# Kernel tuning notes

Measured on AMD Instinct MI355X. Metric: run time of the kernel, lower is better.

Reference implementation:

```python
import jax, jax.numpy as jnp
import numpy as np

_PADE_B = np.array([6.476475253248e+16, 3.238237626624e+16, 7771770303897600.0,
                    1187353796428800.0, 129060195264000.0, 10559470521600.0,
                    670442572800.0, 33522128640.0, 1323241920.0, 40840800.0,
                    960960.0, 16380.0, 182.0, 1.0])
_MAXNORM = 5.371920351148152
_MAX_SQUARINGS = 6  # randn 3x3 has Fro norm ~3 < maxnorm; 6 steps is ample headroom


def _expm(A):
    """Batched scaling-and-squaring Pade-13 matrix exponential. A: [N, d, d]."""
    b = _PADE_B.astype(A.dtype)
    d = A.shape[-1]
    ident = jnp.eye(d, dtype=A.dtype)
    fro = jnp.sqrt(jnp.sum(A * A, axis=(1, 2), keepdims=True))  # [N,1,1]
    n_sq = jnp.maximum(0.0, jnp.ceil(jnp.log2(fro / _MAXNORM)))
    Ascaled = A / (2.0 ** n_sq)
    n_sq_i = n_sq.reshape(-1).astype(jnp.int32)  # [N]

    A2 = Ascaled @ Ascaled
    A4 = A2 @ A2
    A6 = A4 @ A2
    U = Ascaled @ (A6 @ (b[13] * A6 + b[11] * A4 + b[9] * A2)
                   + b[7] * A6 + b[5] * A4 + b[3] * A2 + b[1] * ident)
    V = (A6 @ (b[12] * A6 + b[10] * A4 + b[8] * A2)
         + b[6] * A6 + b[4] * A4 + b[2] * A2 + b[0] * ident)
    P = U + V
    Q = -U + V
    R = jnp.linalg.solve(Q, P)  # torch.solve(P, Q): Q X = P

    def body(k, R):
        R2 = R @ R
        return jnp.where((k < n_sq_i)[:, None, None], R2, R)

    return jax.lax.fori_loop(0, _MAX_SQUARINGS, body, R, unroll=True)


def setup_inputs() -> dict:
    key = jax.random.key(0)
    k1, k2, k3 = jax.random.split(key, 3)
    bs, n, d = 65536, 24, 3
    return {
        "mean": jax.random.normal(k1, (bs, n, d), dtype=jnp.float32),
        "var": jax.random.normal(k2, (bs, n, d, d), dtype=jnp.float32),
        "gt": jax.random.normal(k3, (bs, n, d), dtype=jnp.float32),
    }


def reference(mean, var, gt):
    bs, n, d = mean.shape
    A = var.reshape(bs * n, d, d)
    E = _expm(A)                               # [bs*n, d, d]
    delta = (gt - mean).reshape(bs * n, d)     # [bs*n, d]
    quad = jnp.einsum('ni,nij,nj->n', delta, E, delta)
    dets = jnp.linalg.det(A)
    per = 0.5 * (quad + dets) / n              # [bs*n]
    loss = per.reshape(bs, n).sum(axis=1)      # [bs]
    return loss.mean()
```

## Files before the change

### kernel.cpp

```cpp
#include <hip/hip_runtime.h>

#define TPB 256

#define B0  6.476475253248e+16f
#define B1  3.238237626624e+16f
#define B2  7.7717703038976e+15f
#define B3  1.1873537964288e+15f
#define B4  1.29060195264e+14f
#define B5  1.05594705216e+13f
#define B6  6.704425728e+11f
#define B7  3.352212864e+10f
#define B8  1.32324192e+9f
#define B9  4.08408e+7f
#define B10 9.6096e+5f
#define B11 1.638e+4f
#define B12 182.0f
#define B13 1.0f

__device__ __forceinline__ void mm3(const float a[9], const float b[9], float c[9]) {
#pragma unroll
  for (int i = 0; i < 3; ++i) {
#pragma unroll
    for (int j = 0; j < 3; ++j) {
      c[i * 3 + j] = fmaf(a[i * 3 + 0], b[0 + j],
                     fmaf(a[i * 3 + 1], b[3 + j],
                          a[i * 3 + 2] * b[6 + j]));
    }
  }
}

__global__ __launch_bounds__(TPB, 4) void expm_loss_kernel(
    const float* __restrict__ mean, const float* __restrict__ var,
    const float* __restrict__ gt, float* __restrict__ partials) {
  const int tid = threadIdx.x;
  const long long i = (long long)blockIdx.x * TPB + tid;

  const float* av = var + i * 9;
  const float* mv = mean + i * 3;
  const float* gv = gt + i * 3;

  float A[9];
#pragma unroll
  for (int k = 0; k < 9; ++k) A[k] = av[k];
  const float d0 = gv[0] - mv[0];
  const float d1 = gv[1] - mv[1];
  const float d2 = gv[2] - mv[2];

  const float detA = A[0] * (A[4] * A[8] - A[5] * A[7])
                   - A[1] * (A[3] * A[8] - A[5] * A[6])
                   + A[2] * (A[3] * A[7] - A[4] * A[6]);
  float fro2 = 0.f;
#pragma unroll
  for (int k = 0; k < 9; ++k) fro2 = fmaf(A[k], A[k], fro2);
  const float nsqf = fmaxf(0.0f, ceilf(fmaf(0.5f, __log2f(fro2), -2.4253625f)));
  int nsq = (int)nsqf;
  nsq = nsq > 6 ? 6 : nsq;
  const float scl = exp2f(-nsqf);

  float As[9];
#pragma unroll
  for (int k = 0; k < 9; ++k) As[k] = A[k] * scl;

  float A2[9], A4[9], A6[9];
  mm3(As, As, A2);
  mm3(A2, A2, A4);
  mm3(A4, A2, A6);

  float W[9], T[9], U[9], V[9];
#pragma unroll
  for (int k = 0; k < 9; ++k)
    W[k] = fmaf(B13, A6[k], fmaf(B11, A4[k], B9 * A2[k]));
  mm3(A6, W, T);
#pragma unroll
  for (int k = 0; k < 9; ++k)
    T[k] = fmaf(B7, A6[k], fmaf(B5, A4[k], fmaf(B3, A2[k], T[k])));
  T[0] += B1; T[4] += B1; T[8] += B1;
  mm3(As, T, U);

#pragma unroll
  for (int k = 0; k < 9; ++k)
    W[k] = fmaf(B12, A6[k], fmaf(B10, A4[k], B8 * A2[k]));
  mm3(A6, W, V);
#pragma unroll
  for (int k = 0; k < 9; ++k)
    V[k] = fmaf(B6, A6[k], fmaf(B4, A4[k], fmaf(B2, A2[k], V[k])));
  V[0] += B0; V[4] += B0; V[8] += B0;

  const float s = 1.0f / B0;
  float P[9], Q[9];
#pragma unroll
  for (int k = 0; k < 9; ++k) {
    P[k] = (U[k] + V[k]) * s;
    Q[k] = (V[k] - U[k]) * s;
  }

  const float c00 = Q[4] * Q[8] - Q[5] * Q[7];
  const float c01 = Q[5] * Q[6] - Q[3] * Q[8];
  const float c02 = Q[3] * Q[7] - Q[4] * Q[6];
  const float c10 = Q[2] * Q[7] - Q[1] * Q[8];
  const float c11 = Q[0] * Q[8] - Q[2] * Q[6];
  const float c12 = Q[1] * Q[6] - Q[0] * Q[7];
  const float c20 = Q[1] * Q[5] - Q[2] * Q[4];
  const float c21 = Q[2] * Q[3] - Q[0] * Q[5];
  const float c22 = Q[0] * Q[4] - Q[1] * Q[3];
  const float detQ = Q[0] * c00 + Q[1] * c01 + Q[2] * c02;
  const float inv = 1.0f / detQ;
  const float Qi[9] = { c00 * inv, c10 * inv, c20 * inv,
                        c01 * inv, c11 * inv, c21 * inv,
                        c02 * inv, c12 * inv, c22 * inv };
  float R[9];
  mm3(Qi, P, R);

  for (int k = 0; k < nsq; ++k) {
    float R2[9];
    mm3(R, R, R2);
#pragma unroll
    for (int j = 0; j < 9; ++j) R[j] = R2[j];
  }

  const float t0 = fmaf(R[0], d0, fmaf(R[1], d1, R[2] * d2));
  const float t1 = fmaf(R[3], d0, fmaf(R[4], d1, R[5] * d2));
  const float t2 = fmaf(R[6], d0, fmaf(R[7], d1, R[8] * d2));
  const float quad = fmaf(d0, t0, fmaf(d1, t1, d2 * t2));

  float val = 0.5f * (quad + detA);

#pragma unroll
  for (int off = 32; off > 0; off >>= 1) val += __shfl_down(val, off, 64);
  __shared__ float wsum[TPB / 64];
  if ((tid & 63) == 0) wsum[tid >> 6] = val;
  __syncthreads();
  if (tid == 0) {
    float b = 0.f;
#pragma unroll
    for (int w = 0; w < TPB / 64; ++w) b += wsum[w];
    partials[blockIdx.x] = b;
  }
}

#define RTPB 1024
__global__ __launch_bounds__(RTPB) void reduce_partials_kernel(
    const float* __restrict__ partials, int n, double inv_total,
    float* __restrict__ out) {
  double s = 0.0;
  for (int i = threadIdx.x; i < n; i += RTPB) s += (double)partials[i];
#pragma unroll
  for (int off = 32; off > 0; off >>= 1) s += __shfl_down(s, off, 64);
  __shared__ double ds[RTPB / 64];
  if ((threadIdx.x & 63) == 0) ds[threadIdx.x >> 6] = s;
  __syncthreads();
  if (threadIdx.x == 0) {
    double b = 0.0;
#pragma unroll
    for (int w = 0; w < RTPB / 64; ++w) b += ds[w];
    out[0] = (float)(b * inv_total);
  }
}

extern "C" void kernel_launch(void* const* d_in, const int* in_sizes, int n_in,
                              void* d_out, int out_size, void* d_ws, size_t ws_size,
                              hipStream_t stream) {
  const float* mean = (const float*)d_in[0];
  const float* var  = (const float*)d_in[1];
  const float* gt   = (const float*)d_in[2];
  const int nmat    = in_sizes[1] / 9;
  const int nblocks = nmat / TPB;
  float* partials   = (float*)d_ws;

  expm_loss_kernel<<<nblocks, TPB, 0, stream>>>(mean, var, gt, partials);
  reduce_partials_kernel<<<1, RTPB, 0, stream>>>(partials, nblocks,
                                                 1.0 / (double)nmat,
                                                 (float*)d_out);
}
```

Measured before the change: 29.59 us.

## Evaluate Pade polynomials via Cayley-Hamilton scalar recurrences and vectorize var loads

Replaces the 3x3 matrix products for A4, A6 and the Pade U/V polynomials with scalar coefficient recurrences from the Cayley-Hamilton theorem, so every power of the scaled matrix becomes p*B^2+q*B+r*I. This uses the trace, the second invariant and the (already computed) determinant. It also loads the 9-float matrix with three float4 loads plus selects, and swaps the reciprocal for hardware rcp with one Newton step. The goal is to cut ALU work in a compute-bound kernel. The cost is possible numerical differences from the invariant-based recurrences, plus somewhat unusual, possibly misaligned float4 reads near the buffer end.

```diff
diff --git a/kernel.cpp b/kernel.cpp
--- a/kernel.cpp
+++ b/kernel.cpp
@@ -2,20 +2,20 @@
 
 #define TPB 256
 
-#define B0  6.476475253248e+16f
-#define B1  3.238237626624e+16f
-#define B2  7.7717703038976e+15f
-#define B3  1.1873537964288e+15f
-#define B4  1.29060195264e+14f
-#define B5  1.05594705216e+13f
-#define B6  6.704425728e+11f
-#define B7  3.352212864e+10f
-#define B8  1.32324192e+9f
-#define B9  4.08408e+7f
-#define B10 9.6096e+5f
-#define B11 1.638e+4f
-#define B12 182.0f
-#define B13 1.0f
+#define B0c  6.476475253248e+16f
+#define B1c  3.238237626624e+16f
+#define B2c  7.7717703038976e+15f
+#define B3c  1.1873537964288e+15f
+#define B4c  1.29060195264e+14f
+#define B5c  1.05594705216e+13f
+#define B6c  6.704425728e+11f
+#define B7c  3.352212864e+10f
+#define B8c  1.32324192e+9f
+#define B9c  4.08408e+7f
+#define B10c 9.6096e+5f
+#define B11c 1.638e+4f
+#define B12c 182.0f
+#define B13c 1.0f
 
 __device__ __forceinline__ void mm3(const float a[9], const float b[9], float c[9]) {
 #pragma unroll
@@ -35,16 +35,27 @@
   const int tid = threadIdx.x;
   const long long i = (long long)blockIdx.x * TPB + tid;
 
-  const float* av = var + i * 9;
+  const long long e9 = i * 9;
+  const long long b4 = e9 >> 2;
+  const int off = (int)(e9 & 3);
+  const float4* v4 = (const float4*)var;
+  const float4 w0 = v4[b4], w1 = v4[b4 + 1], w2 = v4[b4 + 2];
   const float* mv = mean + i * 3;
   const float* gv = gt + i * 3;
-
+  const float m0 = mv[0], m1 = mv[1], m2 = mv[2];
+  const float g0 = gv[0], g1 = gv[1], g2 = gv[2];
+
+  const float w[12] = {w0.x, w0.y, w0.z, w0.w, w1.x, w1.y, w1.z, w1.w,
+                       w2.x, w2.y, w2.z, w2.w};
+  const bool o1 = (off & 1), o2 = (off & 2);
   float A[9];
 #pragma unroll
-  for (int k = 0; k < 9; ++k) A[k] = av[k];
-  const float d0 = gv[0] - mv[0];
-  const float d1 = gv[1] - mv[1];
-  const float d2 = gv[2] - mv[2];
+  for (int k = 0; k < 9; ++k) {
+    const float a = o1 ? w[k + 1] : w[k];
+    const float b = o1 ? w[k + 3] : w[k + 2];
+    A[k] = o2 ? b : a;
+  }
+  const float d0 = g0 - m0, d1 = g1 - m1, d2 = g2 - m2;
 
   const float detA = A[0] * (A[4] * A[8] - A[5] * A[7])
                    - A[1] * (A[3] * A[8] - A[5] * A[6])
@@ -57,59 +68,81 @@
   nsq = nsq > 6 ? 6 : nsq;
   const float scl = exp2f(-nsqf);
 
-  float As[9];
-#pragma unroll
-  for (int k = 0; k < 9; ++k) As[k] = A[k] * scl;
-
-  float A2[9], A4[9], A6[9];
-  mm3(As, As, A2);
-  mm3(A2, A2, A4);
-  mm3(A4, A2, A6);
-
-  float W[9], T[9], U[9], V[9];
-#pragma unroll
-  for (int k = 0; k < 9; ++k)
-    W[k] = fmaf(B13, A6[k], fmaf(B11, A4[k], B9 * A2[k]));
-  mm3(A6, W, T);
-#pragma unroll
-  for (int k = 0; k < 9; ++k)
-    T[k] = fmaf(B7, A6[k], fmaf(B5, A4[k], fmaf(B3, A2[k], T[k])));
-  T[0] += B1; T[4] += B1; T[8] += B1;
-  mm3(As, T, U);
-
-#pragma unroll
-  for (int k = 0; k < 9; ++k)
-    W[k] = fmaf(B12, A6[k], fmaf(B10, A4[k], B8 * A2[k]));
-  mm3(A6, W, V);
-#pragma unroll
-  for (int k = 0; k < 9; ++k)
-    V[k] = fmaf(B6, A6[k], fmaf(B4, A4[k], fmaf(B2, A2[k], V[k])));
-  V[0] += B0; V[4] += B0; V[8] += B0;
-
-  const float s = 1.0f / B0;
-  float P[9], Q[9];
+  float B[9];
+#pragma unroll
+  for (int k = 0; k < 9; ++k) B[k] = A[k] * scl;
+
+  float B2[9];
+  mm3(B, B, B2);
+
+  const float t = B[0] + B[4] + B[8];
+  const float trB2 = B2[0] + B2[4] + B2[8];
+  const float m = 0.5f * (t * t - trB2);
+  const float dch = detA * scl * scl * scl;
+
+  const float x4p = t * t - m,        x4q = dch - t * m,        x4r = t * dch;
+  const float x5p = fmaf(x4p, t, x4q), x5q = fmaf(-x4p, m, x4r), x5r = x4p * dch;
+  const float x6p = fmaf(x5p, t, x5q), x6q = fmaf(-x5p, m, x5r), x6r = x5p * dch;
+
+  const float w1p = fmaf(B13c, x6p, fmaf(B11c, x4p, B9c));
+  const float w1q = fmaf(B13c, x6q, B11c * x4q);
+  const float w1r = fmaf(B13c, x6r, B11c * x4r);
+  {
+  }
+  const float s4a = x6p * w1p;
+  const float s3a = fmaf(x6p, w1q, x6q * w1p);
+  const float gp = fmaf(s4a, x4p, fmaf(s3a, t,   fmaf(x6p, w1r, fmaf(x6r, w1p, x6q * w1q))));
+  const float gq = fmaf(s4a, x4q, fmaf(s3a, -m,  fmaf(x6q, w1r, x6r * w1q)));
+  const float gr = fmaf(s4a, x4r, fmaf(s3a, dch, x6r * w1r));
+  const float uep = fmaf(B7c, x6p, fmaf(B5c, x4p, gp)) + B3c;
+  const float ueq = fmaf(B7c, x6q, fmaf(B5c, x4q, gq));
+  const float uer = fmaf(B7c, x6r, fmaf(B5c, x4r, gr)) + B1c;
+  const float up = fmaf(uep, t, ueq);
+  const float uq = fmaf(-uep, m, uer);
+  const float ur = uep * dch;
+
+  const float w2p = fmaf(B12c, x6p, fmaf(B10c, x4p, B8c));
+  const float w2q = fmaf(B12c, x6q, B10c * x4q);
+  const float w2r = fmaf(B12c, x6r, B10c * x4r);
+  const float s4b = x6p * w2p;
+  const float s3b = fmaf(x6p, w2q, x6q * w2p);
+  const float hp = fmaf(s4b, x4p, fmaf(s3b, t,   fmaf(x6p, w2r, fmaf(x6r, w2p, x6q * w2q))));
+  const float hq = fmaf(s4b, x4q, fmaf(s3b, -m,  fmaf(x6q, w2r, x6r * w2q)));
+  const float hr = fmaf(s4b, x4r, fmaf(s3b, dch, x6r * w2r));
+  const float vp = fmaf(B6c, x6p, fmaf(B4c, x4p, hp)) + B2c;
+  const float vq = fmaf(B6c, x6q, fmaf(B4c, x4q, hq));
+  const float vr = fmaf(B6c, x6r, fmaf(B4c, x4r, hr)) + B0c;
+
+  const float s = 1.0f / B0c;
+  const float pp = (vp + up) * s, pq = (vq + uq) * s, pr = (vr + ur) * s;
+  const float qp = (vp - up) * s, qq = (vq - uq) * s, qr = (vr - ur) * s;
+
+  float Pm[9], Qm[9];
 #pragma unroll
   for (int k = 0; k < 9; ++k) {
-    P[k] = (U[k] + V[k]) * s;
-    Q[k] = (V[k] - U[k]) * s;
-  }
-
-  const float c00 = Q[4] * Q[8] - Q[5] * Q[7];
-  const float c01 = Q[5] * Q[6] - Q[3] * Q[8];
-  const float c02 = Q[3] * Q[7] - Q[4] * Q[6];
-  const float c10 = Q[2] * Q[7] - Q[1] * Q[8];
-  const float c11 = Q[0] * Q[8] - Q[2] * Q[6];
-  const float c12 = Q[1] * Q[6] - Q[0] * Q[7];
-  const float c20 = Q[1] * Q[5] - Q[2] * Q[4];
-  const float c21 = Q[2] * Q[3] - Q[0] * Q[5];
-  const float c22 = Q[0] * Q[4] - Q[1] * Q[3];
-  const float detQ = Q[0] * c00 + Q[1] * c01 + Q[2] * c02;
-  const float inv = 1.0f / detQ;
+    Pm[k] = fmaf(pp, B2[k], pq * B[k]);
+    Qm[k] = fmaf(qp, B2[k], qq * B[k]);
+  }
+  Pm[0] += pr; Pm[4] += pr; Pm[8] += pr;
+  Qm[0] += qr; Qm[4] += qr; Qm[8] += qr;
+
+  const float c00 = Qm[4] * Qm[8] - Qm[5] * Qm[7];
+  const float c01 = Qm[5] * Qm[6] - Qm[3] * Qm[8];
+  const float c02 = Qm[3] * Qm[7] - Qm[4] * Qm[6];
+  const float c10 = Qm[2] * Qm[7] - Qm[1] * Qm[8];
+  const float c11 = Qm[0] * Qm[8] - Qm[2] * Qm[6];
+  const float c12 = Qm[1] * Qm[6] - Qm[0] * Qm[7];
+  const float c20 = Qm[1] * Qm[5] - Qm[2] * Qm[4];
+  const float c21 = Qm[2] * Qm[3] - Qm[0] * Qm[5];
+  const float c22 = Qm[0] * Qm[4] - Qm[1] * Qm[3];
+  const float detQ = Qm[0] * c00 + Qm[1] * c01 + Qm[2] * c02;
+  float inv = __builtin_amdgcn_rcpf(detQ);
+  inv = inv * (2.0f - detQ * inv);
   const float Qi[9] = { c00 * inv, c10 * inv, c20 * inv,
                         c01 * inv, c11 * inv, c21 * inv,
                         c02 * inv, c12 * inv, c22 * inv };
   float R[9];
-  mm3(Qi, P, R);
+  mm3(Qi, Pm, R);
 
   for (int k = 0; k < nsq; ++k) {
     float R2[9];
@@ -126,14 +159,14 @@
   float val = 0.5f * (quad + detA);
 
 #pragma unroll
-  for (int off = 32; off > 0; off >>= 1) val += __shfl_down(val, off, 64);
+  for (int offx = 32; offx > 0; offx >>= 1) val += __shfl_down(val, offx, 64);
   __shared__ float wsum[TPB / 64];
   if ((tid & 63) == 0) wsum[tid >> 6] = val;
   __syncthreads();
   if (tid == 0) {
     float b = 0.f;
 #pragma unroll
-    for (int w = 0; w < TPB / 64; ++w) b += wsum[w];
+    for (int wi = 0; wi < TPB / 64; ++wi) b += wsum[wi];
     partials[blockIdx.x] = b;
   }
 }
```

Result: slower. 48.74 us (+64.7%).
